# Kernel optimization log

Hardware: AMD Instinct MI355X
Metric: run time of the kernel (lower is better)

Reference implementation:

```python
import jax, jax.numpy as jnp
import numpy as np

B, S, DIN, DH, HN, CHUNK = 8, 8192, 512, 512, 4, 16
HD = DH // HN
LN_EPS = 1e-5
CLAMP = 1e-6


def setup_inputs() -> dict:
    key = jax.random.key(0)
    ks = jax.random.split(key, 8)
    x = jax.random.normal(ks[0], (B, S, DIN), jnp.float32)
    h = jax.random.normal(ks[1], (B, DH), jnp.float32)
    s_in = 1.0 / np.sqrt(DIN)
    W_in = jax.random.uniform(ks[2], (DH, DIN), jnp.float32, -s_in, s_in)
    ln_gamma = jnp.ones((DH,), jnp.float32)
    ln_beta = jnp.zeros((DH,), jnp.float32)
    s_h = 1.0 / np.sqrt(DH)
    W_gate = jax.random.uniform(ks[3], (2 * HN, DH), jnp.float32, -s_h, s_h)
    b_gate = jax.random.uniform(ks[4], (2 * HN,), jnp.float32, -s_h, s_h)
    # raw = atanh(0.9) as in _init_eigenvalues
    eig_raw = jnp.full((HN,), 0.5 * np.log(1.9 / 0.1), jnp.float32)
    W_out = jax.random.uniform(ks[5], (DH, DH), jnp.float32, -s_h, s_h)
    return {"x": x, "h": h, "W_in": W_in, "ln_gamma": ln_gamma, "ln_beta": ln_beta,
            "W_gate": W_gate, "b_gate": b_gate, "eig_raw": eig_raw, "W_out": W_out}


def _forward(x, h, W_in, ln_gamma, ln_beta, W_gate, b_gate, eig_raw, W_out):
    # input projection (no bias) + layernorm
    xp = jnp.einsum('bsi,hi->bsh', x, W_in)
    mu = xp.mean(-1, keepdims=True)
    var = xp.var(-1, keepdims=True)  # biased var, matches torch LayerNorm
    xn = (xp - mu) / jnp.sqrt(var + LN_EPS) * ln_gamma + ln_beta
    # gates
    gates = jnp.einsum('bsh,gh->bsg', xn, W_gate) + b_gate
    alpha = jax.nn.sigmoid(gates[..., :HN])   # (B,S,HN)
    beta = jax.nn.sigmoid(gates[..., HN:])    # (B,S,HN)
    eig = jnp.tanh(eig_raw)                   # (HN,)
    a = eig[None, None, :] * alpha            # (B,S,HN)
    xh = xn.reshape(B, S, HN, HD)
    b = beta[..., None] * xh                  # (B,S,HN,HD)
    h0 = h.reshape(B, HN, HD)
    # chunked parallel scan: h_t = a_t * h_{t-1} + b_t
    nc = S // CHUNK
    a_c = a.reshape(B, nc, CHUNK, HN).transpose(1, 0, 2, 3)          # (nc,B,C,HN)
    b_c = b.reshape(B, nc, CHUNK, HN, HD).transpose(1, 0, 2, 3, 4)   # (nc,B,C,HN,HD)

    def step(hc, ab):
        ac, bc = ab
        cum_a = jnp.cumprod(ac, axis=1)                      # (B,C,HN)
        cum_a_safe = jnp.maximum(cum_a, CLAMP)[..., None]    # clamp(min=1e-6)
        first = cum_a[..., None] * hc[:, None]               # (B,C,HN,HD)
        second = cum_a_safe * jnp.cumsum(bc / cum_a_safe, axis=1)
        h_chunk = first + second
        return h_chunk[:, -1], h_chunk

    _, outs = jax.lax.scan(step, h0, (a_c, b_c))             # outs: (nc,B,C,HN,HD)
    h_all = outs.transpose(1, 0, 2, 3, 4).reshape(B, S, DH)
    out = jnp.einsum('bsh,oh->bso', h_all, W_out)            # dropout is identity (eval)
    return out, h_all[:, -1, :]


def reference(x, h, W_in, ln_gamma, ln_beta, W_gate, b_gate, eig_raw, W_out):
    return _forward(x, h, W_in, ln_gamma, ln_beta, W_gate, b_gate, eig_raw, W_out)
```

## Files before the change

### kernel.cpp

```cpp
#include <hip/hip_runtime.h>
#include <hip/hip_bf16.h>
#include <math.h>

#define B_    8
#define S_    8192
#define DIN_  512
#define DH_   512
#define HN_   4
#define HD_   128
#define CHUNK_ 16
#define NC_   (S_/CHUNK_)
#define NTOK  (B_*S_)

typedef __bf16 bf16x8 __attribute__((ext_vector_type(8)));
typedef float  f32x4  __attribute__((ext_vector_type(4)));

__device__ __forceinline__ float sigmoidf_(float z) { return 1.0f / (1.0f + expf(-z)); }

__device__ __forceinline__ unsigned short f2bf(float f) {
    union { float f; unsigned u; } v; v.f = f;
    unsigned u = v.u;
    u += 0x7fffu + ((u >> 16) & 1u);
    return (unsigned short)(u >> 16);
}
__device__ __forceinline__ float bf2f(unsigned short s) {
    union { unsigned u; float f; } c; c.u = ((unsigned)s) << 16; return c.f;
}
__device__ __forceinline__ unsigned long long pack4bf(float4 a) {
    union { __bf16 h[4]; unsigned long long u; } c;
    c.h[0] = (__bf16)a.x; c.h[1] = (__bf16)a.y;
    c.h[2] = (__bf16)a.z; c.h[3] = (__bf16)a.w;
    return c.u;
}
__device__ __forceinline__ void gload_lds16(const void* g, void* lds) {
    __builtin_amdgcn_global_load_lds(
        (const __attribute__((address_space(1))) unsigned int*)g,
        (__attribute__((address_space(3))) unsigned int*)lds, 16, 0, 0);
}

#define AOFF(og, r) ((((og) << 11) + ((r) << 4)) ^ ((og) << 5))
#define BOFF(og, c) (((og) << 11) + ((c) << 4))

#define XCD_DECODE(mt, ct)                        \
    const int _bid = blockIdx.x;                  \
    const int _j = _bid >> 3;                     \
    const int mt = ((_j >> 2) << 3) + (_bid & 7); \
    const int ct = _j & 3;

__global__ __launch_bounds__(256) void k0_convert(
    const float* __restrict__ Win, const float* __restrict__ Wout,
    unsigned short* __restrict__ WreA, unsigned short* __restrict__ WreB)
{
    int idx = blockIdx.x * 256 + threadIdx.x;
    if (idx < 262144) {
        int c_g = idx >> 9, k = idx & 511;
        int dst = ((((c_g >> 7) * 16 + (k >> 5)) * 4 + ((k >> 3) & 3)) << 10)
                + ((c_g & 127) << 3) + (k & 7);
        WreA[dst] = f2bf(Win[idx]);
        WreB[dst] = f2bf(Wout[idx]);
    }
}

__global__ __launch_bounds__(256, 4) void gemm1(
    const float* __restrict__ x, const unsigned short* __restrict__ Wre,
    unsigned short* __restrict__ xpb)
{
    __shared__ alignas(16) unsigned short Bl[8192];
    __shared__ alignas(16) unsigned short Al[8192];
    char* Blc = (char*)Bl; char* Alc = (char*)Al;
    const int tid = threadIdx.x;
    const int l = tid & 63, wid = tid >> 6;
    const int og = l >> 4, lr = l & 15;
    const int wr = wid >> 1, wc2 = wid & 1;
    XCD_DECODE(mt, ct)
    const long t0 = (long)mt * 128;
    const int c0 = ct << 7;
    const int r0 = tid >> 2, ogk = tid & 3;

    f32x4 acc[4][4];
    #pragma unroll
    for (int m = 0; m < 4; ++m)
        #pragma unroll
        for (int n = 0; n < 4; ++n) acc[m][n] = (f32x4)(0.f);

    for (int kt2 = 0; kt2 < 8; ++kt2) {
        __syncthreads();
        #pragma unroll
        for (int s = 0; s < 2; ++s) {
            const int kt = (kt2 << 1) + s;
            const char* gB = (const char*)Wre + ((long)(ct * 16 + kt) << 13);
            char* BlS = Blc + (s << 13);
            gload_lds16(gB + (wid << 10) + (l << 4),        BlS + (wid << 10));
            gload_lds16(gB + 4096 + (wid << 10) + (l << 4), BlS + 4096 + (wid << 10));
            const int kb = kt << 5;
            const float* xr0 = &x[(t0 + r0) * 512 + kb + (ogk << 3)];
            const float* xr1 = &x[(t0 + r0 + 64) * 512 + kb + (ogk << 3)];
            float4 a0 = *(const float4*)xr0, a1 = *(const float4*)(xr0 + 4);
            float4 b0 = *(const float4*)xr1, b1 = *(const float4*)(xr1 + 4);
            ulonglong2 w0, w1;
            w0.x = pack4bf(a0); w0.y = pack4bf(a1);
            w1.x = pack4bf(b0); w1.y = pack4bf(b1);
            char* AlS = Alc + (s << 13);
            *(ulonglong2*)(AlS + AOFF(ogk, r0))      = w0;
            *(ulonglong2*)(AlS + AOFF(ogk, r0 + 64)) = w1;
        }
        __syncthreads();

        #pragma unroll
        for (int s = 0; s < 2; ++s) {
            const char* AlS = Alc + (s << 13);
            const char* BlS = Blc + (s << 13);
            bf16x8 afr[4], bfr[4];
            #pragma unroll
            for (int m = 0; m < 4; ++m)
                afr[m] = *(const bf16x8*)(AlS + AOFF(og, (wr << 6) + (m << 4) + lr));
            #pragma unroll
            for (int n = 0; n < 4; ++n)
                bfr[n] = *(const bf16x8*)(BlS + BOFF(og, (wc2 << 6) + (n << 4) + lr));
            #pragma unroll
            for (int m = 0; m < 4; ++m)
                #pragma unroll
                for (int n = 0; n < 4; ++n)
                    acc[m][n] = __builtin_amdgcn_mfma_f32_16x16x32_bf16(afr[m], bfr[n], acc[m][n], 0, 0, 0);
        }
    }

    #pragma unroll
    for (int m = 0; m < 4; ++m) {
        const long rb = t0 + (wr << 6) + (m << 4) + (og << 2);
        #pragma unroll
        for (int n = 0; n < 4; ++n) {
            const int col = c0 + (wc2 << 6) + (n << 4) + lr;
            #pragma unroll
            for (int j = 0; j < 4; ++j)
                xpb[(rb + j) * 512 + col] = f2bf(acc[m][n][j]);
        }
    }
}

__global__ __launch_bounds__(256) void k_lnA(
    const unsigned short* __restrict__ xpb,
    const float* __restrict__ gamma, const float* __restrict__ beta,
    const float* __restrict__ Wg, const float* __restrict__ bg,
    const float* __restrict__ eig_raw,
    unsigned short* __restrict__ A2, float* __restrict__ B15,
    float* __restrict__ p_buf)
{
    __shared__ float bnS[16][512];
    __shared__ float WgL[8][512];
    __shared__ float qS[16][4];
    __shared__ float rqS[16][4];
    __shared__ float aS[16][4];

    const int tid = threadIdx.x;
    const int l = tid & 63, w = tid >> 6;
    const int lg = l >> 4;
    const int li = l & 15;
    const int r  = (w << 2) + lg;
    const long t0 = (long)blockIdx.x * 16;
    const long tok = t0 + r;

    float4 v[8];
    #pragma unroll
    for (int jj = 0; jj < 8; ++jj) {
        const ushort4 u = *(const ushort4*)&xpb[tok * 512 + (jj << 6) + (li << 2)];
        v[jj] = make_float4(bf2f(u.x), bf2f(u.y), bf2f(u.z), bf2f(u.w));
    }

    #pragma unroll
    for (int i = 0; i < 4; ++i)
        ((float4*)WgL)[tid + 256 * i] = ((const float4*)Wg)[tid + 256 * i];
    __syncthreads();

    float s1 = 0.f, s2 = 0.f;
    #pragma unroll
    for (int jj = 0; jj < 8; ++jj) {
        s1 += v[jj].x + v[jj].y + v[jj].z + v[jj].w;
        s2 += v[jj].x*v[jj].x + v[jj].y*v[jj].y + v[jj].z*v[jj].z + v[jj].w*v[jj].w;
    }
    #pragma unroll
    for (int o = 1; o < 16; o <<= 1) { s1 += __shfl_xor(s1, o, 64); s2 += __shfl_xor(s2, o, 64); }
    const float mean = s1 * (1.f/512.f);
    const float var  = s2 * (1.f/512.f) - mean*mean;
    const float rstd = 1.0f / sqrtf(var + 1e-5f);

    #pragma unroll
    for (int jj = 0; jj < 8; ++jj) {
        const float4 g = *(const float4*)&gamma[(jj << 6) + (li << 2)];
        const float4 b = *(const float4*)&beta[(jj << 6) + (li << 2)];
        v[jj].x = (v[jj].x - mean)*rstd*g.x + b.x;
        v[jj].y = (v[jj].y - mean)*rstd*g.y + b.y;
        v[jj].z = (v[jj].z - mean)*rstd*g.z + b.z;
        v[jj].w = (v[jj].w - mean)*rstd*g.w + b.w;
    }

    float gt[8];
    #pragma unroll
    for (int g = 0; g < 8; ++g) {
        float p = 0.f;
        #pragma unroll
        for (int jj = 0; jj < 8; ++jj) {
            const float4 wv = *(const float4*)&WgL[g][(jj << 6) + (li << 2)];
            p = fmaf(v[jj].x, wv.x, p); p = fmaf(v[jj].y, wv.y, p);
            p = fmaf(v[jj].z, wv.z, p); p = fmaf(v[jj].w, wv.w, p);
        }
        #pragma unroll
        for (int o = 1; o < 16; o <<= 1) p += __shfl_xor(p, o, 64);
        gt[g] = p + bg[g];
    }

    const float bt[4] = {sigmoidf_(gt[4]), sigmoidf_(gt[5]), sigmoidf_(gt[6]), sigmoidf_(gt[7])};
    #pragma unroll
    for (int jj = 0; jj < 8; ++jj) {
        const float b = bt[jj >> 1];
        *(float4*)&bnS[r][(jj << 6) + (li << 2)] =
            make_float4(b*v[jj].x, b*v[jj].y, b*v[jj].z, b*v[jj].w);
    }
    if (li < 4) aS[r][li] = tanhf(eig_raw[li]) * sigmoidf_(gt[li]);
    __syncthreads();

    if (tid < 4) {
        const int n = tid;
        float p = 1.f;
        #pragma unroll
        for (int t = 0; t < 16; ++t) {
            p *= aS[t][n];
            p_buf[(t0 + t) * 4 + n] = p;
            const float q = fmaxf(p, 1e-6f);
            qS[t][n] = q;
            rqS[t][n] = 1.0f / q;
        }
    }
    __syncthreads();

    #pragma unroll
    for (int cc = 0; cc < 2; ++cc) {
        const int c = tid + (cc << 8);
        const int n = c >> 7;
        float s = 0.f;
        #pragma unroll
        for (int t = 0; t < 16; ++t) {
            s = fmaf(bnS[t][c], rqS[t][n], s);
            const float vv = qS[t][n] * s;
            bnS[t][c] = vv;
            if (t == 15) B15[blockIdx.x * 512 + c] = vv;
        }
    }
    __syncthreads();

    const long mtb = t0 >> 7;
    #pragma unroll
    for (int i = 0; i < 4; ++i) {
        const int slot = (i << 8) + tid;
        const int t = slot >> 6, oct = slot & 63;
        const float4 va = *(const float4*)&bnS[t][oct << 3];
        const float4 vb = *(const float4*)&bnS[t][(oct << 3) + 4];
        const int rr = (int)((t0 + t) & 127);
        const long idx = (((mtb * 16 + (oct >> 2)) * 4 + (oct & 3)) << 10) + (rr << 3);
        ulonglong2 wv; wv.x = pack4bf(va); wv.y = pack4bf(vb);
        *(ulonglong2*)&A2[idx] = wv;
    }
}

__global__ __launch_bounds__(256) void k3a_compose(
    const float* __restrict__ p_buf, const float* __restrict__ B15,
    float* __restrict__ Pg, float* __restrict__ Qg)
{
    const int gid = blockIdx.x * 256 + threadIdx.x;
    const int c = gid & 511, g = (gid >> 9) & 31, b = gid >> 14;
    const int n = c >> 7;
    float P = 1.f, Q = 0.f;
    #pragma unroll
    for (int j = 0; j < 16; ++j) {
        const int ch = (g << 4) + j;
        const long gc = (long)b * NC_ + ch;
        const long sE = (long)b * S_ + (long)ch * CHUNK_ + (CHUNK_ - 1);
        const float p15 = p_buf[sE * HN_ + n];
        const float b15 = B15[gc * 512 + c];
        P *= p15;
        Q = fmaf(p15, Q, b15);
    }
    Pg[(long)gid] = P;
    Qg[(long)gid] = Q;
}

__global__ __launch_bounds__(256) void k3b_scan(
    const float* __restrict__ Pg, const float* __restrict__ Qg,
    const float* __restrict__ h_in, float* __restrict__ h0g,
    float* __restrict__ h_last)
{
    const int tid = blockIdx.x * blockDim.x + threadIdx.x;
    const int b = tid >> 9, c = tid & 511;
    float h = h_in[b * DH_ + c];
    for (int g = 0; g < 32; ++g) {
        const long i = ((long)(b * 32 + g)) * 512 + c;
        h0g[i] = h;
        h = fmaf(Pg[i], h, Qg[i]);
    }
    h_last[b * DH_ + c] = h;
}

__global__ __launch_bounds__(256) void k3c_expand(
    const float* __restrict__ p_buf, const float* __restrict__ B15,
    const float* __restrict__ h0g, float* __restrict__ h0_buf)
{
    const int gid = blockIdx.x * 256 + threadIdx.x;
    const int c = gid & 511, g = (gid >> 9) & 31, b = gid >> 14;
    const int n = c >> 7;
    float h = h0g[(long)gid];
    #pragma unroll
    for (int j = 0; j < 16; ++j) {
        const int ch = (g << 4) + j;
        const long gc = (long)b * NC_ + ch;
        h0_buf[gc * 512 + c] = h;
        const long sE = (long)b * S_ + (long)ch * CHUNK_ + (CHUNK_ - 1);
        h = fmaf(p_buf[sE * HN_ + n], h, B15[gc * 512 + c]);
    }
}

__global__ __launch_bounds__(256) void kG(
    const float* __restrict__ h0, const unsigned short* __restrict__ Wre,
    float* __restrict__ G)
{
    __shared__ alignas(16) unsigned short Bl[8192];
    __shared__ alignas(16) unsigned short Al[8192];
    char* Blc = (char*)Bl; char* Alc = (char*)Al;
    const int tid = threadIdx.x;
    const int l = tid & 63, wid = tid >> 6;
    const int og = l >> 4, lr = l & 15;
    const int wr = wid >> 1, wc2 = wid & 1;
    const int ct = blockIdx.x & 3, mt = (blockIdx.x >> 2) & 31, hn = blockIdx.x >> 7;
    const long g0 = (long)mt * 128;
    const int c0 = ct << 7;
    const int r0 = tid >> 2, ogk = tid & 3;

    f32x4 acc[4][4];
    #pragma unroll
    for (int m = 0; m < 4; ++m)
        #pragma unroll
        for (int n = 0; n < 4; ++n) acc[m][n] = (f32x4)(0.f);

    for (int kt2 = 0; kt2 < 2; ++kt2) {
        __syncthreads();
        #pragma unroll
        for (int s = 0; s < 2; ++s) {
            const int kt = (hn << 2) + (kt2 << 1) + s;
            const char* gB = (const char*)Wre + ((long)(ct * 16 + kt) << 13);
            char* BlS = Blc + (s << 13);
            gload_lds16(gB + (wid << 10) + (l << 4),        BlS + (wid << 10));
            gload_lds16(gB + 4096 + (wid << 10) + (l << 4), BlS + 4096 + (wid << 10));
            const int kb = kt << 5;
            const float* xr0 = &h0[(g0 + r0) * 512 + kb + (ogk << 3)];
            const float* xr1 = &h0[(g0 + r0 + 64) * 512 + kb + (ogk << 3)];
            float4 a0 = *(const float4*)xr0, a1 = *(const float4*)(xr0 + 4);
            float4 b0 = *(const float4*)xr1, b1 = *(const float4*)(xr1 + 4);
            ulonglong2 w0, w1;
            w0.x = pack4bf(a0); w0.y = pack4bf(a1);
            w1.x = pack4bf(b0); w1.y = pack4bf(b1);
            char* AlS = Alc + (s << 13);
            *(ulonglong2*)(AlS + AOFF(ogk, r0))      = w0;
            *(ulonglong2*)(AlS + AOFF(ogk, r0 + 64)) = w1;
        }
        __syncthreads();

        #pragma unroll
        for (int s = 0; s < 2; ++s) {
            const char* AlS = Alc + (s << 13);
            const char* BlS = Blc + (s << 13);
            bf16x8 afr[4], bfr[4];
            #pragma unroll
            for (int m = 0; m < 4; ++m)
                afr[m] = *(const bf16x8*)(AlS + AOFF(og, (wr << 6) + (m << 4) + lr));
            #pragma unroll
            for (int n = 0; n < 4; ++n)
                bfr[n] = *(const bf16x8*)(BlS + BOFF(og, (wc2 << 6) + (n << 4) + lr));
            #pragma unroll
            for (int m = 0; m < 4; ++m)
                #pragma unroll
                for (int n = 0; n < 4; ++n)
                    acc[m][n] = __builtin_amdgcn_mfma_f32_16x16x32_bf16(afr[m], bfr[n], acc[m][n], 0, 0, 0);
        }
    }

    float* Gh = G + ((long)hn << 21);
    #pragma unroll
    for (int m = 0; m < 4; ++m) {
        const long rb = g0 + (wr << 6) + (m << 4) + (og << 2);
        #pragma unroll
        for (int n = 0; n < 4; ++n) {
            const int col = c0 + (wc2 << 6) + (n << 4) + lr;
            #pragma unroll
            for (int j = 0; j < 4; ++j)
                Gh[(rb + j) * 512 + col] = acc[m][n][j];
        }
    }
}

__global__ __launch_bounds__(256) void gemm2(
    const unsigned short* __restrict__ A2, const unsigned short* __restrict__ Wre,
    const float* __restrict__ G, const float* __restrict__ p_buf,
    float* __restrict__ out)
{
    __shared__ alignas(16) unsigned short Bl[8192];
    __shared__ alignas(16) unsigned short Al[8192];
    __shared__ float pS[512];
    char* Blc = (char*)Bl; char* Alc = (char*)Al;
    const int tid = threadIdx.x;
    const int l = tid & 63, wid = tid >> 6;
    const int og = l >> 4, lr = l & 15;
    const int wr = wid >> 1, wc2 = wid & 1;
    XCD_DECODE(mt, ct)
    const long t0 = (long)mt * 128;
    const int c0 = ct << 7;

    pS[tid]       = p_buf[t0 * 4 + tid];
    pS[tid + 256] = p_buf[t0 * 4 + 256 + tid];

    f32x4 acc[4][4];
    #pragma unroll
    for (int m = 0; m < 4; ++m)
        #pragma unroll
        for (int n = 0; n < 4; ++n) acc[m][n] = (f32x4)(0.f);

    for (int kt2 = 0; kt2 < 8; ++kt2) {
        __syncthreads();
        #pragma unroll
        for (int s = 0; s < 2; ++s) {
            const int kt = (kt2 << 1) + s;
            const char* gB = (const char*)Wre + ((long)(ct * 16 + kt) << 13);
            const char* gA = (const char*)A2 + ((long)(mt * 16 + kt) << 13);
            char* BlS = Blc + (s << 13);
            char* AlS = Alc + (s << 13);
            gload_lds16(gB + (wid << 10) + (l << 4),        BlS + (wid << 10));
            gload_lds16(gB + 4096 + (wid << 10) + (l << 4), BlS + 4096 + (wid << 10));
            gload_lds16(gA + (wid << 10) + (l << 4),        AlS + (wid << 10));
            gload_lds16(gA + 4096 + (wid << 10) + (l << 4), AlS + 4096 + (wid << 10));
        }
        __syncthreads();

        #pragma unroll
        for (int s = 0; s < 2; ++s) {
            const char* AlS = Alc + (s << 13);
            const char* BlS = Blc + (s << 13);
            bf16x8 afr[4], bfr[4];
            #pragma unroll
            for (int m = 0; m < 4; ++m)
                afr[m] = *(const bf16x8*)(AlS + BOFF(og, (wr << 6) + (m << 4) + lr));
            #pragma unroll
            for (int n = 0; n < 4; ++n)
                bfr[n] = *(const bf16x8*)(BlS + BOFF(og, (wc2 << 6) + (n << 4) + lr));
            #pragma unroll
            for (int m = 0; m < 4; ++m)
                #pragma unroll
                for (int n = 0; n < 4; ++n)
                    acc[m][n] = __builtin_amdgcn_mfma_f32_16x16x32_bf16(afr[m], bfr[n], acc[m][n], 0, 0, 0);
        }
    }

    #pragma unroll
    for (int m = 0; m < 4; ++m) {
        const long gcm = (t0 >> 4) + (wr << 2) + m;
        #pragma unroll
        for (int n = 0; n < 4; ++n) {
            const int col = c0 + (wc2 << 6) + (n << 4) + lr;
            const float g0v = G[gcm * 512 + col];
            const float g1v = G[(1L << 21) + gcm * 512 + col];
            const float g2v = G[(2L << 21) + gcm * 512 + col];
            const float g3v = G[(3L << 21) + gcm * 512 + col];
            #pragma unroll
            for (int j = 0; j < 4; ++j) {
                const int rl = (wr << 6) + (m << 4) + (og << 2) + j;
                const float add = pS[rl*4]*g0v + pS[rl*4+1]*g1v + pS[rl*4+2]*g2v + pS[rl*4+3]*g3v;
                out[(t0 + rl) * 512 + col] = acc[m][n][j] + add;
            }
        }
    }
}

extern "C" void kernel_launch(void* const* d_in, const int* in_sizes, int n_in,
                              void* d_out, int out_size, void* d_ws, size_t ws_size,
                              hipStream_t stream) {
    const float* x       = (const float*)d_in[0];
    const float* h       = (const float*)d_in[1];
    const float* Win     = (const float*)d_in[2];
    const float* gamma   = (const float*)d_in[3];
    const float* beta    = (const float*)d_in[4];
    const float* Wg      = (const float*)d_in[5];
    const float* bg      = (const float*)d_in[6];
    const float* eig_raw = (const float*)d_in[7];
    const float* Wout    = (const float*)d_in[8];

    float* out    = (float*)d_out;
    float* h_last = out + (long)NTOK * DH_;
    unsigned short* xpb = (unsigned short*)d_out;

    float* ws     = (float*)d_ws;
    float* p_buf  = ws;
    float* h0_buf = ws + 262144;
    float* B15    = ws + 2359296;
    float* G      = ws + 4456448;
    unsigned short* WreA = (unsigned short*)(ws + 12845056);
    unsigned short* WreB = WreA + 262144;
    unsigned short* A2   = (unsigned short*)(ws + 13107200);

    float* Pg  = G;
    float* Qg  = G + 131072;
    float* h0g = G + 262144;

    k0_convert<<<1024, 256, 0, stream>>>(Win, Wout, WreA, WreB);
    gemm1<<<2048, 256, 0, stream>>>(x, WreA, xpb);
    k_lnA<<<NTOK/16, 256, 0, stream>>>(xpb, gamma, beta, Wg, bg, eig_raw,
                                       A2, B15, p_buf);
    k3a_compose<<<512, 256, 0, stream>>>(p_buf, B15, Pg, Qg);
    k3b_scan<<<16, 256, 0, stream>>>(Pg, Qg, h, h0g, h_last);
    k3c_expand<<<512, 256, 0, stream>>>(p_buf, B15, h0g, h0_buf);
    kG<<<512, 256, 0, stream>>>(h0_buf, WreB, G);
    gemm2<<<2048, 256, 0, stream>>>(A2, WreB, G, p_buf, out);
}
```

Before: 209.6 us.

## Triple-buffer gemm2 LDS tiles with async prefetch two K-steps ahead

Replaces the load-then-compute loop in the output GEMM (two K slices per barrier pair) with a three-stage ring of LDS buffers. Loads for step kt+2 are issued while step kt computes, and explicit vmcnt waits plus one barrier per step control ordering. The goal is to hide global-to-LDS latency behind the MFMA work and cut the number of barriers. In exchange it uses slightly more LDS (48KB vs 32KB), which may reduce occupancy, and it relies on hand-written waitcnt counts for correctness.

```diff
diff --git a/kernel.cpp b/kernel.cpp
--- a/kernel.cpp
+++ b/kernel.cpp
@@ -401,10 +401,9 @@
     const float* __restrict__ G, const float* __restrict__ p_buf,
     float* __restrict__ out)
 {
-    __shared__ alignas(16) unsigned short Bl[8192];
-    __shared__ alignas(16) unsigned short Al[8192];
+    __shared__ alignas(16) unsigned short Bl[3][4096];
+    __shared__ alignas(16) unsigned short Al[3][4096];
     __shared__ float pS[512];
-    char* Blc = (char*)Bl; char* Alc = (char*)Al;
     const int tid = threadIdx.x;
     const int l = tid & 63, wid = tid >> 6;
     const int og = l >> 4, lr = l & 15;
@@ -415,6 +414,21 @@
 
     pS[tid]       = p_buf[t0 * 4 + tid];
     pS[tid + 256] = p_buf[t0 * 4 + 256 + tid];
+    __syncthreads();
+
+    const char* gBbase = (const char*)Wre + ((long)(ct * 16) << 13);
+    const char* gAbase = (const char*)A2  + ((long)(mt * 16) << 13);
+    const int src_off = (wid << 10) + (l << 4);
+    const int dst_off = (wid << 10);
+
+#define STAGE2(kt, buf) do {                                               \
+        const char* gB_ = gBbase + ((long)(kt) << 13);                     \
+        const char* gA_ = gAbase + ((long)(kt) << 13);                     \
+        gload_lds16(gB_ + src_off,        (char*)Bl[buf] + dst_off);       \
+        gload_lds16(gB_ + 4096 + src_off, (char*)Bl[buf] + 4096 + dst_off);\
+        gload_lds16(gA_ + src_off,        (char*)Al[buf] + dst_off);       \
+        gload_lds16(gA_ + 4096 + src_off, (char*)Al[buf] + 4096 + dst_off);\
+    } while (0)
 
     f32x4 acc[4][4];
     #pragma unroll
@@ -422,40 +436,33 @@
         #pragma unroll
         for (int n = 0; n < 4; ++n) acc[m][n] = (f32x4)(0.f);
 
-    for (int kt2 = 0; kt2 < 8; ++kt2) {
-        __syncthreads();
-        #pragma unroll
-        for (int s = 0; s < 2; ++s) {
-            const int kt = (kt2 << 1) + s;
-            const char* gB = (const char*)Wre + ((long)(ct * 16 + kt) << 13);
-            const char* gA = (const char*)A2 + ((long)(mt * 16 + kt) << 13);
-            char* BlS = Blc + (s << 13);
-            char* AlS = Alc + (s << 13);
-            gload_lds16(gB + (wid << 10) + (l << 4),        BlS + (wid << 10));
-            gload_lds16(gB + 4096 + (wid << 10) + (l << 4), BlS + 4096 + (wid << 10));
-            gload_lds16(gA + (wid << 10) + (l << 4),        AlS + (wid << 10));
-            gload_lds16(gA + 4096 + (wid << 10) + (l << 4), AlS + 4096 + (wid << 10));
-        }
-        __syncthreads();
-
-        #pragma unroll
-        for (int s = 0; s < 2; ++s) {
-            const char* AlS = Alc + (s << 13);
-            const char* BlS = Blc + (s << 13);
-            bf16x8 afr[4], bfr[4];
-            #pragma unroll
-            for (int m = 0; m < 4; ++m)
-                afr[m] = *(const bf16x8*)(AlS + BOFF(og, (wr << 6) + (m << 4) + lr));
+    STAGE2(0, 0);
+    STAGE2(1, 1);
+
+    #pragma unroll
+    for (int kt = 0; kt < 16; ++kt) {
+        if (kt < 15) asm volatile("s_waitcnt vmcnt(4) lgkmcnt(0)" ::: "memory");
+        else         asm volatile("s_waitcnt vmcnt(0) lgkmcnt(0)" ::: "memory");
+        __builtin_amdgcn_s_barrier();
+        asm volatile("" ::: "memory");
+        if (kt < 14) STAGE2(kt + 2, (kt + 2) % 3);
+
+        const char* AlS = (const char*)Al[kt % 3];
+        const char* BlS = (const char*)Bl[kt % 3];
+        bf16x8 afr[4], bfr[4];
+        #pragma unroll
+        for (int m = 0; m < 4; ++m)
+            afr[m] = *(const bf16x8*)(AlS + BOFF(og, (wr << 6) + (m << 4) + lr));
+        #pragma unroll
+        for (int n = 0; n < 4; ++n)
+            bfr[n] = *(const bf16x8*)(BlS + BOFF(og, (wc2 << 6) + (n << 4) + lr));
+        #pragma unroll
+        for (int m = 0; m < 4; ++m)
             #pragma unroll
             for (int n = 0; n < 4; ++n)
-                bfr[n] = *(const bf16x8*)(BlS + BOFF(og, (wc2 << 6) + (n << 4) + lr));
-            #pragma unroll
-            for (int m = 0; m < 4; ++m)
-                #pragma unroll
-                for (int n = 0; n < 4; ++n)
-                    acc[m][n] = __builtin_amdgcn_mfma_f32_16x16x32_bf16(afr[m], bfr[n], acc[m][n], 0, 0, 0);
-        }
-    }
+                acc[m][n] = __builtin_amdgcn_mfma_f32_16x16x32_bf16(afr[m], bfr[n], acc[m][n], 0, 0, 0);
+    }
+#undef STAGE2
 
     #pragma unroll
     for (int m = 0; m < 4; ++m) {
```

Result: no change. 210.3 us (+0.3%).
